# Optimization experiments

Hardware: AMD Instinct MI355X
Metric: run time of the kernel (lower is better)

## Reference

```python
import jax, jax.numpy as jnp
import numpy as np

B, H, W = 8, 160, 160
L = H * W  # 25600, matches nn.LayerNorm(25600)
QDIM = KDIM = MID = OUT = 256
HEADS = 8
HEAD_DIM = MID // HEADS  # 32
LN_EPS = 1e-5


def conv1x1(x, w, b):
    # x: [N,C,H,W], w: [O,C], b: [O] -> [N,O,H,W]
    return jnp.einsum('nchw,oc->nohw', x, w) + b[None, :, None, None]


def setup_inputs() -> dict:
    key = jax.random.key(0)
    ks = jax.random.split(key, 12)
    s = 0.02
    return {
        'query': jax.random.normal(ks[0], (B, QDIM, H, W), jnp.float32),
        'key': jax.random.normal(ks[1], (B, KDIM, H, W), jnp.float32),
        'Wq': jax.random.normal(ks[2], (MID, QDIM), jnp.float32) * s,
        'bq': jnp.zeros((MID,), jnp.float32),
        'Wk': jax.random.normal(ks[3], (MID, KDIM), jnp.float32) * s,
        'bk': jnp.zeros((MID,), jnp.float32),
        'Wv': jax.random.normal(ks[4], (MID, KDIM), jnp.float32) * s,
        'bv': jnp.zeros((MID,), jnp.float32),
        'Wo': jax.random.normal(ks[5], (OUT, MID), jnp.float32) * s,
        'bo': jnp.zeros((OUT,), jnp.float32),
        'gamma': jnp.ones((L,), jnp.float32),
        'beta': jnp.zeros((L,), jnp.float32),
    }


def reference(query, key, Wq, bq, Wk, bk, Wv, bv, Wo, bo, gamma, beta):
    # 1x1-conv projections, flatten spatial dims to L
    q = conv1x1(query, Wq, bq).reshape(B, HEADS, HEAD_DIM, L)
    k = conv1x1(key, Wk, bk).reshape(B, HEADS, HEAD_DIM, L)
    v = conv1x1(key, Wv, bv).reshape(B, HEADS, HEAD_DIM, L)
    # NOTE: faithful to the source, scores contract over L (spatial), giving
    # a [B, heads, head_dim, head_dim] channel-attention matrix.
    scores = jnp.einsum('nhdl,nhel->nhde', q, k) / (KDIM ** 0.5)
    attn = jax.nn.softmax(scores, axis=-1)  # dropout is identity at eval
    out = jnp.einsum('nhde,nhel->nhdl', attn, v).reshape(B, MID, L)
    # LayerNorm over the flattened spatial axis (size 25600)
    mu = jnp.mean(out, axis=-1, keepdims=True)
    var = jnp.var(out, axis=-1, keepdims=True)
    out = (out - mu) * jax.lax.rsqrt(var + LN_EPS) * gamma + beta
    out = out.reshape(B, MID, H, W)
    return conv1x1(out, Wo, bo)
```

## Files before the change

### kernel.cpp

```cpp
#include <hip/hip_runtime.h>
#include <hip/hip_bf16.h>
#include <stdint.h>

#define LROW 25600
#define NCH 256
#define LN_EPS 1e-5f

typedef float f32x4 __attribute__((ext_vector_type(4)));
typedef __bf16 bf16x8 __attribute__((ext_vector_type(8)));
typedef __bf16 bf16x4 __attribute__((ext_vector_type(4)));
typedef uint32_t u32x2 __attribute__((ext_vector_type(2)));

__device__ __forceinline__ bf16x8 cvt8(f32x4 a, f32x4 b) {
  bf16x8 r;
  r[0] = (__bf16)a[0]; r[1] = (__bf16)a[1]; r[2] = (__bf16)a[2]; r[3] = (__bf16)a[3];
  r[4] = (__bf16)b[0]; r[5] = (__bf16)b[1]; r[6] = (__bf16)b[2]; r[7] = (__bf16)b[3];
  return r;
}

__device__ __forceinline__ void wg_bar() {
  asm volatile("s_waitcnt lgkmcnt(0)\n\ts_barrier" ::: "memory");
}

template <int FULL>
__global__ __launch_bounds__(1024, 4) void gram_k(
    const float* __restrict__ qg, const float* __restrict__ kg,
    float* __restrict__ Gd, float* __restrict__ Gkkd,
    float* __restrict__ sq, float* __restrict__ sk,
    __bf16* __restrict__ kbf) {
  __shared__ __align__(16) __bf16 lA[256 * 32];
  __shared__ __align__(16) __bf16 lB[256 * 32];
  const int bid = blockIdx.x;
  const int b = bid >> 5, s = bid & 31;
  const int mat = (s < 21) ? 0 : 1;
  const int idx = mat ? (s - 21) : s;
  const int parts = mat ? 11 : 21;
  const int c0 = (800 * idx) / parts, c1 = (800 * (idx + 1)) / parts;
  const int nc = c1 - c0;
  const int tid = threadIdx.x;
  const int w = tid >> 6, lane = tid & 63;
  const int wr = w >> 2, wc = w & 3;
  const int lr = lane & 15, g = lane >> 4;
  const float* Ag = (mat ? kg : qg) + (size_t)b * NCH * LROW;
  const float* Bg = kg + (size_t)b * NCH * LROW;

  const int rowS = tid >> 2, uS = tid & 3;
  const int uSw = uS ^ ((rowS >> 1) & 3);
  const size_t gOff = (size_t)rowS * LROW + uS * 8;
  __bf16* ldsA_dst = lA + rowS * 32 + uSw * 8;
  __bf16* ldsB_dst = lB + rowS * 32 + uSw * 8;

  const f32x4 zero = {0.f, 0.f, 0.f, 0.f};
  f32x4 acc[4][4];
#pragma unroll
  for (int i = 0; i < 4; ++i)
#pragma unroll
    for (int j = 0; j < 4; ++j) acc[i][j] = zero;

  float rsum = 0.f;

  auto LOADG = [&](int c, f32x4* d) {
    const float* pa = Ag + gOff + (size_t)c * 32;
    d[0] = *(const f32x4*)pa;
    d[1] = *(const f32x4*)(pa + 4);
    if (mat == 0) {
      const float* pb = Bg + gOff + (size_t)c * 32;
      d[2] = *(const f32x4*)pb;
      d[3] = *(const f32x4*)(pb + 4);
    }
  };

  auto PROCESS = [&](int c, f32x4* d) {
#pragma unroll
    for (int e = 0; e < 4; ++e) rsum += d[0][e] + d[1][e];
    bf16x8 av = cvt8(d[0], d[1]);
    *(bf16x8*)ldsA_dst = av;
    if (mat == 0) {
      *(bf16x8*)ldsB_dst = cvt8(d[2], d[3]);
    } else if (FULL) {
      *(bf16x8*)(kbf + (size_t)(b * NCH + rowS) * LROW + (size_t)c * 32 + uS * 8) = av;
    }
    wg_bar();
    const __bf16* Bp = mat ? lA : lB;
    bf16x8 af[4];
#pragma unroll
    for (int i = 0; i < 4; ++i) {
      const int row = wr * 64 + i * 16 + lr;
      const int u = g ^ ((row >> 1) & 3);
      af[i] = *(const bf16x8*)(lA + row * 32 + u * 8);
    }
#pragma unroll
    for (int j = 0; j < 4; ++j) {
      const int row = wc * 64 + j * 16 + lr;
      const int u = g ^ ((row >> 1) & 3);
      bf16x8 bfj = *(const bf16x8*)(Bp + row * 32 + u * 8);
#pragma unroll
      for (int i = 0; i < 4; ++i)
        acc[i][j] = __builtin_amdgcn_mfma_f32_16x16x32_bf16(af[i], bfj, acc[i][j], 0, 0, 0);
    }
    wg_bar();
  };

  f32x4 bA[4], bB[4];
  LOADG(c0, bA);
  int cc = 0;
  for (; cc + 2 <= nc; cc += 2) {
    LOADG(c0 + cc + 1, bB);
    PROCESS(c0 + cc, bA);
    if (cc + 2 < nc) LOADG(c0 + cc + 2, bA);
    PROCESS(c0 + cc + 1, bB);
  }
  if (cc < nc) PROCESS(c0 + cc, bA);

  atomicAdd((mat ? sk : sq) + b * NCH + rowS, rsum);

  if (FULL) {
    float* Gout = mat ? (Gkkd + ((size_t)b * 11 + idx) * 65536)
                      : (Gd + ((size_t)b * 21 + idx) * 65536);
#pragma unroll
    for (int i = 0; i < 4; ++i)
#pragma unroll
      for (int j = 0; j < 4; ++j) {
        const int col = wc * 64 + j * 16 + lr;
        const int row0 = wr * 64 + i * 16 + g * 4;
#pragma unroll
        for (int r = 0; r < 4; ++r)
          Gout[(size_t)(row0 + r) * NCH + col] = acc[i][j][r];
      }
  } else {
    float* Gout = (mat ? Gkkd : Gd) + (size_t)b * 65536;
#pragma unroll
    for (int i = 0; i < 4; ++i)
#pragma unroll
      for (int j = 0; j < 4; ++j) {
        const int col = wc * 64 + j * 16 + lr;
        const int row0 = wr * 64 + i * 16 + g * 4;
#pragma unroll
        for (int r = 0; r < 4; ++r)
          atomicAdd(&Gout[(size_t)(row0 + r) * NCH + col], acc[i][j][r]);
      }
  }
}

__global__ __launch_bounds__(256) void reduce_k(
    const float* __restrict__ Gp, const float* __restrict__ Gkkp,
    float* __restrict__ Gred, float* __restrict__ Gkkred) {
  const f32x4 zero = {0.f, 0.f, 0.f, 0.f};
  if (blockIdx.x < 512) {
    int f = (blockIdx.x * 256 + threadIdx.x) * 4;
    int b = f >> 16, r = f & 65535;
    f32x4 a = zero;
    for (int si = 0; si < 21; ++si)
      a += *(const f32x4*)(Gp + ((size_t)b * 21 + si) * 65536 + r);
    *(f32x4*)(Gred + f) = a;
  } else {
    int f = ((blockIdx.x - 512) * 256 + threadIdx.x) * 4;
    int b = f >> 16, r = f & 65535;
    f32x4 a = zero;
    for (int si = 0; si < 11; ++si)
      a += *(const f32x4*)(Gkkp + ((size_t)b * 11 + si) * 65536 + r);
    *(f32x4*)(Gkkred + f) = a;
  }
}

__global__ __launch_bounds__(256) void attn_k(
    const float* __restrict__ G, const float* __restrict__ sq,
    const float* __restrict__ sk,
    const float* __restrict__ Wq, const float* __restrict__ bq,
    const float* __restrict__ Wk, const float* __restrict__ bk,
    const float* __restrict__ Wv, const float* __restrict__ bv,
    float* __restrict__ M, float* __restrict__ cvec) {
  __shared__ float Wql[32][257];
  __shared__ float Wkl[32][257];
  __shared__ float QGl[32][257];
  __shared__ float Sl[32][33];
  __shared__ float Al[32][33];
  __shared__ float ul[32], wl[32];
  const int b = blockIdx.x >> 3, h = blockIdx.x & 7;
  const int t = threadIdx.x;
  const float* Gb = G + (size_t)b * 65536;

  for (int i = 0; i < 32; ++i) {
    int idx = i * 256 + t;
    int d = idx >> 8, c = idx & 255;
    Wql[d][c] = Wq[(h * 32 + d) * 256 + c];
    Wkl[d][c] = Wk[(h * 32 + d) * 256 + c];
  }
  __syncthreads();
  {
    float a[32];
#pragma unroll
    for (int d = 0; d < 32; ++d) a[d] = 0.f;
    for (int c = 0; c < 256; ++c) {
      float gv = Gb[c * 256 + t];
#pragma unroll
      for (int d = 0; d < 32; ++d) a[d] += Wql[d][c] * gv;
    }
    for (int d = 0; d < 32; ++d) QGl[d][t] = a[d];
  }
  if (t < 32) {
    float u = 0.f, wv = 0.f;
    for (int c = 0; c < 256; ++c) {
      u += Wql[t][c] * sq[b * 256 + c];
      wv += Wkl[t][c] * sk[b * 256 + c];
    }
    ul[t] = u; wl[t] = wv;
  }
  __syncthreads();
  for (int i = 0; i < 4; ++i) {
    int idx = i * 256 + t;
    int d = idx >> 5, e = idx & 31;
    float sv = 0.f;
    for (int c = 0; c < 256; ++c) sv += QGl[d][c] * Wkl[e][c];
    float bqd = bq[h * 32 + d], bke = bk[h * 32 + e];
    Sl[d][e] = (sv + ul[d] * bke + bqd * wl[e] + 25600.f * bqd * bke) * (1.f / 16.f);
  }
  __syncthreads();
  if (t < 32) {
    float m = -1e30f;
    for (int e = 0; e < 32; ++e) m = fmaxf(m, Sl[t][e]);
    float ssum = 0.f;
    for (int e = 0; e < 32; ++e) { float p = __expf(Sl[t][e] - m); Al[t][e] = p; ssum += p; }
    float is = 1.f / ssum;
    for (int e = 0; e < 32; ++e) Al[t][e] *= is;
  }
  __syncthreads();
  {
    float a[32];
#pragma unroll
    for (int d = 0; d < 32; ++d) a[d] = 0.f;
    for (int e = 0; e < 32; ++e) {
      float wv = Wv[(h * 32 + e) * 256 + t];
#pragma unroll
      for (int d = 0; d < 32; ++d) a[d] += Al[d][e] * wv;
    }
    for (int d = 0; d < 32; ++d) M[((size_t)b * 256 + h * 32 + d) * 256 + t] = a[d];
  }
  if (t < 32) {
    float cv = 0.f;
    for (int e = 0; e < 32; ++e) cv += Al[t][e] * bv[h * 32 + e];
    cvec[b * 256 + h * 32 + t] = cv;
  }
}

__global__ __launch_bounds__(256) void stats_k(
    const float* __restrict__ Gkk, const float* __restrict__ M,
    const float* __restrict__ sk, const float* __restrict__ cvec,
    float* __restrict__ mu, float* __restrict__ inv) {
  __shared__ float Ml[32][257];
  __shared__ float Ql[32][257];
  const int b = blockIdx.x >> 3, cb = blockIdx.x & 7;
  const int t = threadIdx.x;
  const float* Gk = Gkk + (size_t)b * 65536;
  for (int i = 0; i < 32; ++i) {
    int idx = i * 256 + t;
    Ml[idx >> 8][idx & 255] = M[((size_t)b * 256 + cb * 32 + (idx >> 8)) * 256 + (idx & 255)];
  }
  __syncthreads();
  {
    float a[32];
#pragma unroll
    for (int c = 0; c < 32; ++c) a[c] = 0.f;
    for (int cc = 0; cc < 256; ++cc) {
      float gv = Gk[cc * 256 + t];
#pragma unroll
      for (int c = 0; c < 32; ++c) a[c] += Ml[c][cc] * gv;
    }
    for (int c = 0; c < 32; ++c) Ql[c][t] = a[c];
  }
  __syncthreads();
  if (t < 32) {
    float qf = 0.f, msk = 0.f;
    for (int j = 0; j < 256; ++j) {
      qf += Ql[t][j] * Ml[t][j];
      msk += Ml[t][j] * sk[b * 256 + j];
    }
    int c = cb * 32 + t;
    float cv = cvec[b * 256 + c];
    float muv = msk * (1.f / 25600.f) + cv;
    float sum2 = qf + 2.f * cv * msk + 25600.f * cv * cv;
    float var = sum2 * (1.f / 25600.f) - muv * muv;
    mu[b * 256 + c] = muv;
    inv[b * 256 + c] = rsqrtf(var + LN_EPS);
  }
}

__global__ __launch_bounds__(256) void pmat_k(
    const float* __restrict__ M, const float* __restrict__ Wo,
    const float* __restrict__ inv, const float* __restrict__ cvec,
    const float* __restrict__ mu, __bf16* __restrict__ Pb,
    float* __restrict__ t1, float* __restrict__ wsum) {
  __shared__ float Wol[32][257];
  __shared__ float invl[256];
  const int b = blockIdx.x >> 3, ob = blockIdx.x & 7;
  const int t = threadIdx.x;
  invl[t] = inv[b * 256 + t];
  __syncthreads();
  for (int i = 0; i < 32; ++i) {
    int idx = i * 256 + t;
    int o = idx >> 8, c = idx & 255;
    Wol[o][c] = Wo[(ob * 32 + o) * 256 + c] * invl[c];
  }
  __syncthreads();
  {
    float a[32];
#pragma unroll
    for (int o = 0; o < 32; ++o) a[o] = 0.f;
    for (int c = 0; c < 256; ++c) {
      float m = M[((size_t)b * 256 + c) * 256 + t];
#pragma unroll
      for (int o = 0; o < 32; ++o) a[o] += Wol[o][c] * m;
    }
    for (int o = 0; o < 32; ++o)
      Pb[((size_t)b * 256 + ob * 32 + o) * 256 + t] = (__bf16)a[o];
  }
  if (t < 32) {
    float s1 = 0.f, s2 = 0.f;
    for (int c = 0; c < 256; ++c) {
      s1 += Wol[t][c] * (cvec[b * 256 + c] - mu[b * 256 + c]);
      s2 += Wo[(ob * 32 + t) * 256 + c];
    }
    t1[b * 256 + ob * 32 + t] = s1;
    wsum[b * 256 + ob * 32 + t] = s2;
  }
}

__global__ __launch_bounds__(512, 4) void outb_k(
    const __bf16* __restrict__ kbf, const __bf16* __restrict__ Pb,
    const float* __restrict__ t1, const float* __restrict__ wsum,
    const float* __restrict__ bo, const float* __restrict__ gamma,
    const float* __restrict__ beta, float* __restrict__ out) {
  __shared__ __align__(16) __bf16 Bt[128 * 256];
  const int bid = blockIdx.x;
  const int b = bid / 200, lt = bid % 200, l0 = lt * 128;
  const int tid = threadIdx.x, w = tid >> 6, lane = tid & 63;
  const int wr = w >> 1, wc = w & 1;
  const int lr = lane & 15, g = lane >> 4;
  const __bf16* Kb = kbf + (size_t)b * NCH * LROW;

#pragma unroll
  for (int i = 0; i < 8; ++i) {
    const int cb = i * 32 + w * 4;
    const __bf16* src = Kb + (size_t)cb * LROW + l0 + lane * 2;
    uint32_t d0 = *(const uint32_t*)src;
    uint32_t d1 = *(const uint32_t*)(src + LROW);
    uint32_t d2 = *(const uint32_t*)(src + 2 * LROW);
    uint32_t d3 = *(const uint32_t*)(src + 3 * LROW);
    u32x2 lo, hi;
    lo[0] = (d0 & 0xffffu) | (d1 << 16);
    lo[1] = (d2 & 0xffffu) | (d3 << 16);
    hi[0] = (d0 >> 16) | (d1 & 0xffff0000u);
    hi[1] = (d2 >> 16) | (d3 & 0xffff0000u);
    const int unit = i * 4 + (w >> 1), sub = (w & 1) * 8;
    const int llo = lane * 2, lhi = llo + 1;
    *(u32x2*)((char*)Bt + llo * 512 + ((unit ^ (llo & 7)) << 4) + sub) = lo;
    *(u32x2*)((char*)Bt + lhi * 512 + ((unit ^ (lhi & 7)) << 4) + sub) = hi;
  }
  __syncthreads();

  const f32x4 zero = {0.f, 0.f, 0.f, 0.f};
  f32x4 acc[4][4];
#pragma unroll
  for (int i = 0; i < 4; ++i)
#pragma unroll
    for (int j = 0; j < 4; ++j) acc[i][j] = zero;

  const __bf16* Pbase = Pb + (size_t)b * 65536;
#pragma unroll
  for (int ks = 0; ks < 8; ++ks) {
    bf16x8 af[4];
#pragma unroll
    for (int i = 0; i < 4; ++i) {
      const int row = wr * 64 + i * 16 + lr;
      af[i] = *(const bf16x8*)(Pbase + (size_t)row * 256 + ks * 32 + g * 8);
    }
#pragma unroll
    for (int j = 0; j < 4; ++j) {
      const int col = wc * 64 + j * 16 + lr;
      const int unit = ks * 4 + g;
      bf16x8 bfj = *(const bf16x8*)((const char*)Bt + col * 512 + ((unit ^ (col & 7)) << 4));
#pragma unroll
      for (int i = 0; i < 4; ++i)
        acc[i][j] = __builtin_amdgcn_mfma_f32_16x16x32_bf16(af[i], bfj, acc[i][j], 0, 0, 0);
    }
  }

  float t1r[4][4], wsr[4][4], bor[4][4];
#pragma unroll
  for (int i = 0; i < 4; ++i)
#pragma unroll
    for (int r = 0; r < 4; ++r) {
      const int row = wr * 64 + i * 16 + g * 4 + r;
      t1r[i][r] = t1[b * 256 + row];
      wsr[i][r] = wsum[b * 256 + row];
      bor[i][r] = bo[row];
    }
#pragma unroll
  for (int j = 0; j < 4; ++j) {
    const int colg = l0 + wc * 64 + j * 16 + lr;
    const float gm = gamma[colg];
    const float bt = beta[colg];
#pragma unroll
    for (int i = 0; i < 4; ++i) {
      const int row0 = wr * 64 + i * 16 + g * 4;
#pragma unroll
      for (int r = 0; r < 4; ++r) {
        const int row = row0 + r;
        float v = gm * (acc[i][j][r] + t1r[i][r]) + bt * wsr[i][r] + bor[i][r];
        out[((size_t)b * 256 + row) * LROW + colg] = v;
      }
    }
  }
}

__global__ __launch_bounds__(512, 2) void out_f32_k(
    const float* __restrict__ key, const __bf16* __restrict__ Pb,
    const float* __restrict__ t1, const float* __restrict__ wsum,
    const float* __restrict__ bo, const float* __restrict__ gamma,
    const float* __restrict__ beta, float* __restrict__ out) {
  __shared__ __align__(16) __bf16 Bt[256 * 256];
  const int bid = blockIdx.x;
  const int b = bid / 100, tt = bid % 100;
  const int l0 = tt * 256;
  const int tid = threadIdx.x, w = tid >> 6, lane = tid & 63;
  const float* Kb = key + (size_t)b * NCH * LROW;

  for (int i = 0; i < 32; ++i) {
    int idx = i * 512 + tid;
    int l = idx & 255, cq = idx >> 8;
    float x0 = Kb[(size_t)(cq * 4 + 0) * LROW + l0 + l];
    float x1 = Kb[(size_t)(cq * 4 + 1) * LROW + l0 + l];
    float x2 = Kb[(size_t)(cq * 4 + 2) * LROW + l0 + l];
    float x3 = Kb[(size_t)(cq * 4 + 3) * LROW + l0 + l];
    bf16x4 hv;
    hv[0] = (__bf16)x0; hv[1] = (__bf16)x1; hv[2] = (__bf16)x2; hv[3] = (__bf16)x3;
    int unit = cq >> 1;
    int byteoff = l * 512 + (((unit ^ (l & 7))) << 4) + (cq & 1) * 8;
    *(bf16x4*)((char*)Bt + byteoff) = hv;
  }
  __syncthreads();

  const int rb = w >> 1, chh = w & 1;
  const f32x4 zero = {0.f, 0.f, 0.f, 0.f};
  f32x4 acc[2][4][4];
#pragma unroll
  for (int t = 0; t < 2; ++t)
#pragma unroll
    for (int i = 0; i < 4; ++i)
#pragma unroll
      for (int j = 0; j < 4; ++j) acc[t][i][j] = zero;

#pragma unroll
  for (int ks = 0; ks < 8; ++ks) {
    bf16x8 a[4];
#pragma unroll
    for (int i = 0; i < 4; ++i) {
      const int row = rb * 64 + i * 16 + (lane & 15);
      a[i] = *(const bf16x8*)(Pb + ((size_t)b * 256 + row) * 256 + ks * 32 + (lane >> 4) * 8);
    }
#pragma unroll
    for (int t = 0; t < 2; ++t) {
#pragma unroll
      for (int j = 0; j < 4; ++j) {
        const int col = chh * 128 + t * 64 + j * 16 + (lane & 15);
        const int unit = ks * 4 + (lane >> 4);
        const int byteoff = col * 512 + ((unit ^ (col & 7)) << 4);
        bf16x8 bfrag = *(const bf16x8*)((const char*)Bt + byteoff);
#pragma unroll
        for (int i = 0; i < 4; ++i)
          acc[t][i][j] = __builtin_amdgcn_mfma_f32_16x16x32_bf16(a[i], bfrag, acc[t][i][j], 0, 0, 0);
      }
    }
  }

  float t1r[4][4], wsr[4][4], bor[4][4];
#pragma unroll
  for (int i = 0; i < 4; ++i)
#pragma unroll
    for (int r = 0; r < 4; ++r) {
      const int row = rb * 64 + i * 16 + (lane >> 4) * 4 + r;
      t1r[i][r] = t1[b * 256 + row];
      wsr[i][r] = wsum[b * 256 + row];
      bor[i][r] = bo[row];
    }
#pragma unroll
  for (int t = 0; t < 2; ++t)
#pragma unroll
    for (int j = 0; j < 4; ++j) {
      const int col = chh * 128 + t * 64 + j * 16 + (lane & 15);
      const float gm = gamma[l0 + col];
      const float bt = beta[l0 + col];
#pragma unroll
      for (int i = 0; i < 4; ++i) {
        const int row0 = rb * 64 + i * 16 + (lane >> 4) * 4;
#pragma unroll
        for (int r = 0; r < 4; ++r) {
          const int row = row0 + r;
          float v = gm * (acc[t][i][j][r] + t1r[i][r]) + bt * wsr[i][r] + bor[i][r];
          out[((size_t)b * 256 + row) * LROW + l0 + col] = v;
        }
      }
    }
}

extern "C" void kernel_launch(void* const* d_in, const int* in_sizes, int n_in,
                              void* d_out, int out_size, void* d_ws, size_t ws_size,
                              hipStream_t stream) {
  const float* query = (const float*)d_in[0];
  const float* key   = (const float*)d_in[1];
  const float* Wq = (const float*)d_in[2];
  const float* bq = (const float*)d_in[3];
  const float* Wk = (const float*)d_in[4];
  const float* bk = (const float*)d_in[5];
  const float* Wv = (const float*)d_in[6];
  const float* bv = (const float*)d_in[7];
  const float* Wo = (const float*)d_in[8];
  const float* bo = (const float*)d_in[9];
  const float* gamma = (const float*)d_in[10];
  const float* beta  = (const float*)d_in[11];
  float* out = (float*)d_out;

  float* ws = (float*)d_ws;
  float* G    = ws;
  float* Gkk  = G + 524288;
  float* sq   = Gkk + 524288;
  float* sk   = sq + 2048;
  float* M    = sk + 2048;
  float* cvec = M + 524288;
  float* mu   = cvec + 2048;
  float* inv  = mu + 2048;
  float* t1   = inv + 2048;
  float* wsum = t1 + 2048;
  __bf16* Pb  = (__bf16*)(wsum + 2048);
  __bf16* kbf = (__bf16*)(wsum + 2048 + 262144);
  float* Gp   = (float*)kbf + 13107200;
  Gp = ws + 28063744;
  float* Gkkp = ws + 39073792;
  const size_t need = (size_t)44840960 * 4;
  const bool full = ws_size >= need;

  if (full) {
    hipMemsetAsync(sq, 0, 4096 * sizeof(float), stream);
    gram_k<1><<<256, 1024, 0, stream>>>(query, key, Gp, Gkkp, sq, sk, kbf);
    reduce_k<<<1024, 256, 0, stream>>>(Gp, Gkkp, G, Gkk);
  } else {
    hipMemsetAsync(d_ws, 0, (size_t)1052672 * sizeof(float), stream);
    gram_k<0><<<256, 1024, 0, stream>>>(query, key, G, Gkk, sq, sk, nullptr);
  }
  attn_k<<<64, 256, 0, stream>>>(G, sq, sk, Wq, bq, Wk, bk, Wv, bv, M, cvec);
  stats_k<<<64, 256, 0, stream>>>(Gkk, M, sk, cvec, mu, inv);
  pmat_k<<<64, 256, 0, stream>>>(M, Wo, inv, cvec, mu, Pb, t1, wsum);
  if (full) {
    outb_k<<<1600, 512, 0, stream>>>(kbf, Pb, t1, wsum, bo, gamma, beta, out);
  } else {
    out_f32_k<<<800, 512, 0, stream>>>(key, Pb, t1, wsum, bo, gamma, beta, out);
  }
}
```

Measured before the change: 673.1 us.

## Drop bf16 key staging and partial-Gram reduce; atomics with XCD-aware block mapping

Removes the path that wrote a bf16 copy of key plus per-slice partial Gram matrices and reduced them in a separate kernel. Gram partials are now atomically accumulated into a zeroed buffer. Blocks are remapped so each XCD (bid&7) gets a balanced mix of batches and slices. The output kernel reads fp32 key directly and converts it to bf16 into LDS with scalar stores. This cuts workspace traffic and one launch, at the cost of float atomics and heavier fp32 key reads in the final GEMM.

```diff
diff --git a/kernel.cpp b/kernel.cpp
--- a/kernel.cpp
+++ b/kernel.cpp
@@ -8,8 +8,6 @@
 
 typedef float f32x4 __attribute__((ext_vector_type(4)));
 typedef __bf16 bf16x8 __attribute__((ext_vector_type(8)));
-typedef __bf16 bf16x4 __attribute__((ext_vector_type(4)));
-typedef uint32_t u32x2 __attribute__((ext_vector_type(2)));
 
 __device__ __forceinline__ bf16x8 cvt8(f32x4 a, f32x4 b) {
   bf16x8 r;
@@ -22,16 +20,30 @@
   asm volatile("s_waitcnt lgkmcnt(0)\n\ts_barrier" ::: "memory");
 }
 
-template <int FULL>
 __global__ __launch_bounds__(1024, 4) void gram_k(
     const float* __restrict__ qg, const float* __restrict__ kg,
     float* __restrict__ Gd, float* __restrict__ Gkkd,
-    float* __restrict__ sq, float* __restrict__ sk,
-    __bf16* __restrict__ kbf) {
+    float* __restrict__ sq, float* __restrict__ sk) {
   __shared__ __align__(16) __bf16 lA[256 * 32];
   __shared__ __align__(16) __bf16 lB[256 * 32];
+
   const int bid = blockIdx.x;
-  const int b = bid >> 5, s = bid & 31;
+  const int x = bid & 7;
+  int n = bid >> 3;
+  int b = 0, s = 0;
+  for (int bb = 0; bb < 8; ++bb) {
+    const int gsl = (x - bb) & 7;
+    const int gs = (21 * gsl + 7) >> 3, ge = (21 * gsl + 28) >> 3;
+    const int ks = (11 * gsl + 7) >> 3, ke = (11 * gsl + 18) >> 3;
+    const int cnt = (ge - gs) + (ke - ks);
+    if (n < cnt) {
+      b = bb;
+      s = (n < ge - gs) ? (gs + n) : (21 + ks + (n - (ge - gs)));
+      break;
+    }
+    n -= cnt;
+  }
+
   const int mat = (s < 21) ? 0 : 1;
   const int idx = mat ? (s - 21) : s;
   const int parts = mat ? 11 : 21;
@@ -70,16 +82,11 @@
     }
   };
 
-  auto PROCESS = [&](int c, f32x4* d) {
+  auto PROCESS = [&](f32x4* d) {
 #pragma unroll
     for (int e = 0; e < 4; ++e) rsum += d[0][e] + d[1][e];
-    bf16x8 av = cvt8(d[0], d[1]);
-    *(bf16x8*)ldsA_dst = av;
-    if (mat == 0) {
-      *(bf16x8*)ldsB_dst = cvt8(d[2], d[3]);
-    } else if (FULL) {
-      *(bf16x8*)(kbf + (size_t)(b * NCH + rowS) * LROW + (size_t)c * 32 + uS * 8) = av;
-    }
+    *(bf16x8*)ldsA_dst = cvt8(d[0], d[1]);
+    if (mat == 0) *(bf16x8*)ldsB_dst = cvt8(d[2], d[3]);
     wg_bar();
     const __bf16* Bp = mat ? lA : lB;
     bf16x8 af[4];
@@ -106,61 +113,25 @@
   int cc = 0;
   for (; cc + 2 <= nc; cc += 2) {
     LOADG(c0 + cc + 1, bB);
-    PROCESS(c0 + cc, bA);
+    PROCESS(bA);
     if (cc + 2 < nc) LOADG(c0 + cc + 2, bA);
-    PROCESS(c0 + cc + 1, bB);
-  }
-  if (cc < nc) PROCESS(c0 + cc, bA);
+    PROCESS(bB);
+  }
+  if (cc < nc) PROCESS(bA);
 
   atomicAdd((mat ? sk : sq) + b * NCH + rowS, rsum);
 
-  if (FULL) {
-    float* Gout = mat ? (Gkkd + ((size_t)b * 11 + idx) * 65536)
-                      : (Gd + ((size_t)b * 21 + idx) * 65536);
-#pragma unroll
-    for (int i = 0; i < 4; ++i)
-#pragma unroll
-      for (int j = 0; j < 4; ++j) {
-        const int col = wc * 64 + j * 16 + lr;
-        const int row0 = wr * 64 + i * 16 + g * 4;
-#pragma unroll
-        for (int r = 0; r < 4; ++r)
-          Gout[(size_t)(row0 + r) * NCH + col] = acc[i][j][r];
-      }
-  } else {
-    float* Gout = (mat ? Gkkd : Gd) + (size_t)b * 65536;
-#pragma unroll
-    for (int i = 0; i < 4; ++i)
-#pragma unroll
-      for (int j = 0; j < 4; ++j) {
-        const int col = wc * 64 + j * 16 + lr;
-        const int row0 = wr * 64 + i * 16 + g * 4;
-#pragma unroll
-        for (int r = 0; r < 4; ++r)
-          atomicAdd(&Gout[(size_t)(row0 + r) * NCH + col], acc[i][j][r]);
-      }
-  }
-}
-
-__global__ __launch_bounds__(256) void reduce_k(
-    const float* __restrict__ Gp, const float* __restrict__ Gkkp,
-    float* __restrict__ Gred, float* __restrict__ Gkkred) {
-  const f32x4 zero = {0.f, 0.f, 0.f, 0.f};
-  if (blockIdx.x < 512) {
-    int f = (blockIdx.x * 256 + threadIdx.x) * 4;
-    int b = f >> 16, r = f & 65535;
-    f32x4 a = zero;
-    for (int si = 0; si < 21; ++si)
-      a += *(const f32x4*)(Gp + ((size_t)b * 21 + si) * 65536 + r);
-    *(f32x4*)(Gred + f) = a;
-  } else {
-    int f = ((blockIdx.x - 512) * 256 + threadIdx.x) * 4;
-    int b = f >> 16, r = f & 65535;
-    f32x4 a = zero;
-    for (int si = 0; si < 11; ++si)
-      a += *(const f32x4*)(Gkkp + ((size_t)b * 11 + si) * 65536 + r);
-    *(f32x4*)(Gkkred + f) = a;
-  }
+  float* Gout = (mat ? Gkkd : Gd) + (size_t)b * 65536;
+#pragma unroll
+  for (int i = 0; i < 4; ++i)
+#pragma unroll
+    for (int j = 0; j < 4; ++j) {
+      const int col = wc * 64 + j * 16 + lr;
+      const int row0 = wr * 64 + i * 16 + g * 4;
+#pragma unroll
+      for (int r = 0; r < 4; ++r)
+        atomicAdd(&Gout[(size_t)(row0 + r) * NCH + col], acc[i][j][r]);
+    }
 }
 
 __global__ __launch_bounds__(256) void attn_k(
@@ -325,8 +296,8 @@
   }
 }
 
-__global__ __launch_bounds__(512, 4) void outb_k(
-    const __bf16* __restrict__ kbf, const __bf16* __restrict__ Pb,
+__global__ __launch_bounds__(512, 4) void outf_k(
+    const float* __restrict__ key, const __bf16* __restrict__ Pb,
     const float* __restrict__ t1, const float* __restrict__ wsum,
     const float* __restrict__ bo, const float* __restrict__ gamma,
     const float* __restrict__ beta, float* __restrict__ out) {
@@ -336,25 +307,21 @@
   const int tid = threadIdx.x, w = tid >> 6, lane = tid & 63;
   const int wr = w >> 1, wc = w & 1;
   const int lr = lane & 15, g = lane >> 4;
-  const __bf16* Kb = kbf + (size_t)b * NCH * LROW;
-
-#pragma unroll
-  for (int i = 0; i < 8; ++i) {
-    const int cb = i * 32 + w * 4;
-    const __bf16* src = Kb + (size_t)cb * LROW + l0 + lane * 2;
-    uint32_t d0 = *(const uint32_t*)src;
-    uint32_t d1 = *(const uint32_t*)(src + LROW);
-    uint32_t d2 = *(const uint32_t*)(src + 2 * LROW);
-    uint32_t d3 = *(const uint32_t*)(src + 3 * LROW);
-    u32x2 lo, hi;
-    lo[0] = (d0 & 0xffffu) | (d1 << 16);
-    lo[1] = (d2 & 0xffffu) | (d3 << 16);
-    hi[0] = (d0 >> 16) | (d1 & 0xffff0000u);
-    hi[1] = (d2 >> 16) | (d3 & 0xffff0000u);
-    const int unit = i * 4 + (w >> 1), sub = (w & 1) * 8;
-    const int llo = lane * 2, lhi = llo + 1;
-    *(u32x2*)((char*)Bt + llo * 512 + ((unit ^ (llo & 7)) << 4) + sub) = lo;
-    *(u32x2*)((char*)Bt + lhi * 512 + ((unit ^ (lhi & 7)) << 4) + sub) = hi;
+  const float* Kb = key + (size_t)b * NCH * LROW;
+
+  {
+    const int c = tid & 255, seg = tid >> 8;
+    const int uc = c >> 3, cb2 = (c & 7) * 2;
+    const float* src = Kb + (size_t)c * LROW + l0 + seg * 64;
+#pragma unroll
+    for (int i = 0; i < 16; ++i) {
+      f32x4 v = *(const f32x4*)(src + i * 4);
+#pragma unroll
+      for (int j = 0; j < 4; ++j) {
+        const int l = seg * 64 + i * 4 + j;
+        *(__bf16*)((char*)Bt + l * 512 + ((uc ^ (l & 7)) << 4) + cb2) = (__bf16)v[j];
+      }
+    }
   }
   __syncthreads();
 
@@ -411,96 +378,6 @@
       }
     }
   }
-}
-
-__global__ __launch_bounds__(512, 2) void out_f32_k(
-    const float* __restrict__ key, const __bf16* __restrict__ Pb,
-    const float* __restrict__ t1, const float* __restrict__ wsum,
-    const float* __restrict__ bo, const float* __restrict__ gamma,
-    const float* __restrict__ beta, float* __restrict__ out) {
-  __shared__ __align__(16) __bf16 Bt[256 * 256];
-  const int bid = blockIdx.x;
-  const int b = bid / 100, tt = bid % 100;
-  const int l0 = tt * 256;
-  const int tid = threadIdx.x, w = tid >> 6, lane = tid & 63;
-  const float* Kb = key + (size_t)b * NCH * LROW;
-
-  for (int i = 0; i < 32; ++i) {
-    int idx = i * 512 + tid;
-    int l = idx & 255, cq = idx >> 8;
-    float x0 = Kb[(size_t)(cq * 4 + 0) * LROW + l0 + l];
-    float x1 = Kb[(size_t)(cq * 4 + 1) * LROW + l0 + l];
-    float x2 = Kb[(size_t)(cq * 4 + 2) * LROW + l0 + l];
-    float x3 = Kb[(size_t)(cq * 4 + 3) * LROW + l0 + l];
-    bf16x4 hv;
-    hv[0] = (__bf16)x0; hv[1] = (__bf16)x1; hv[2] = (__bf16)x2; hv[3] = (__bf16)x3;
-    int unit = cq >> 1;
-    int byteoff = l * 512 + (((unit ^ (l & 7))) << 4) + (cq & 1) * 8;
-    *(bf16x4*)((char*)Bt + byteoff) = hv;
-  }
-  __syncthreads();
-
-  const int rb = w >> 1, chh = w & 1;
-  const f32x4 zero = {0.f, 0.f, 0.f, 0.f};
-  f32x4 acc[2][4][4];
-#pragma unroll
-  for (int t = 0; t < 2; ++t)
-#pragma unroll
-    for (int i = 0; i < 4; ++i)
-#pragma unroll
-      for (int j = 0; j < 4; ++j) acc[t][i][j] = zero;
-
-#pragma unroll
-  for (int ks = 0; ks < 8; ++ks) {
-    bf16x8 a[4];
-#pragma unroll
-    for (int i = 0; i < 4; ++i) {
-      const int row = rb * 64 + i * 16 + (lane & 15);
-      a[i] = *(const bf16x8*)(Pb + ((size_t)b * 256 + row) * 256 + ks * 32 + (lane >> 4) * 8);
-    }
-#pragma unroll
-    for (int t = 0; t < 2; ++t) {
-#pragma unroll
-      for (int j = 0; j < 4; ++j) {
-        const int col = chh * 128 + t * 64 + j * 16 + (lane & 15);
-        const int unit = ks * 4 + (lane >> 4);
-        const int byteoff = col * 512 + ((unit ^ (col & 7)) << 4);
-        bf16x8 bfrag = *(const bf16x8*)((const char*)Bt + byteoff);
-#pragma unroll
-        for (int i = 0; i < 4; ++i)
-          acc[t][i][j] = __builtin_amdgcn_mfma_f32_16x16x32_bf16(a[i], bfrag, acc[t][i][j], 0, 0, 0);
-      }
-    }
-  }
-
-  float t1r[4][4], wsr[4][4], bor[4][4];
-#pragma unroll
-  for (int i = 0; i < 4; ++i)
-#pragma unroll
-    for (int r = 0; r < 4; ++r) {
-      const int row = rb * 64 + i * 16 + (lane >> 4) * 4 + r;
-      t1r[i][r] = t1[b * 256 + row];
-      wsr[i][r] = wsum[b * 256 + row];
-      bor[i][r] = bo[row];
-    }
-#pragma unroll
-  for (int t = 0; t < 2; ++t)
-#pragma unroll
-    for (int j = 0; j < 4; ++j) {
-      const int col = chh * 128 + t * 64 + j * 16 + (lane & 15);
-      const float gm = gamma[l0 + col];
-      const float bt = beta[l0 + col];
-#pragma unroll
-      for (int i = 0; i < 4; ++i) {
-        const int row0 = rb * 64 + i * 16 + (lane >> 4) * 4;
-#pragma unroll
-        for (int r = 0; r < 4; ++r) {
-          const int row = row0 + r;
-          float v = gm * (acc[t][i][j][r] + t1r[i][r]) + bt * wsr[i][r] + bor[i][r];
-          out[((size_t)b * 256 + row) * LROW + l0 + col] = v;
-        }
-      }
-    }
 }
 
 extern "C" void kernel_launch(void* const* d_in, const int* in_sizes, int n_in,
@@ -532,27 +409,12 @@
   float* t1   = inv + 2048;
   float* wsum = t1 + 2048;
   __bf16* Pb  = (__bf16*)(wsum + 2048);
-  __bf16* kbf = (__bf16*)(wsum + 2048 + 262144);
-  float* Gp   = (float*)kbf + 13107200;
-  Gp = ws + 28063744;
-  float* Gkkp = ws + 39073792;
-  const size_t need = (size_t)44840960 * 4;
-  const bool full = ws_size >= need;
-
-  if (full) {
-    hipMemsetAsync(sq, 0, 4096 * sizeof(float), stream);
-    gram_k<1><<<256, 1024, 0, stream>>>(query, key, Gp, Gkkp, sq, sk, kbf);
-    reduce_k<<<1024, 256, 0, stream>>>(Gp, Gkkp, G, Gkk);
-  } else {
-    hipMemsetAsync(d_ws, 0, (size_t)1052672 * sizeof(float), stream);
-    gram_k<0><<<256, 1024, 0, stream>>>(query, key, G, Gkk, sq, sk, nullptr);
-  }
+
+  hipMemsetAsync(d_ws, 0, (size_t)(524288 * 2 + 4096) * sizeof(float), stream);
+
+  gram_k<<<256, 1024, 0, stream>>>(query, key, G, Gkk, sq, sk);
   attn_k<<<64, 256, 0, stream>>>(G, sq, sk, Wq, bq, Wk, bk, Wv, bv, M, cvec);
   stats_k<<<64, 256, 0, stream>>>(Gkk, M, sk, cvec, mu, inv);
   pmat_k<<<64, 256, 0, stream>>>(M, Wo, inv, cvec, mu, Pb, t1, wsum);
-  if (full) {
-    outb_k<<<1600, 512, 0, stream>>>(kbf, Pb, t1, wsum, bo, gamma, beta, out);
-  } else {
-    out_f32_k<<<800, 512, 0, stream>>>(key, Pb, t1, wsum, bo, gamma, beta, out);
-  }
-}
+  outf_k<<<1600, 512, 0, stream>>>(key, Pb, t1, wsum, bo, gamma, beta, out);
+}
```

Result: slower. 707.1 us (+5.1%).
